# Optimization experiments

Hardware: AMD Instinct MI355X
Metric: run time of the kernel (lower is better)

## Reference

```python
import jax, jax.numpy as jnp
import numpy as np

N = 100_000   # num nodes
E = 3_200_000 # num directed edges (before self-loops)
NEG_SLOPE = 0.2


def setup_inputs() -> dict:
    key = jax.random.key(0)
    ks = jax.random.split(key, 12)
    x = jax.random.normal(ks[0], (N, 2), jnp.float32)
    edge_index = jax.random.randint(ks[1], (2, E), 0, N, dtype=jnp.int32)
    # GATConv(2, 16): lin weight [2,16] (no bias), att_src/att_dst [16], out bias [16]
    W1 = jax.random.normal(ks[2], (2, 16), jnp.float32) * (1.0 / np.sqrt(2.0))
    a_src1 = jax.random.normal(ks[3], (16,), jnp.float32) * 0.25
    a_dst1 = jax.random.normal(ks[4], (16,), jnp.float32) * 0.25
    b1 = jnp.zeros((16,), jnp.float32)
    # GATConv(16, 64)
    W2 = jax.random.normal(ks[5], (16, 64), jnp.float32) * (1.0 / np.sqrt(16.0))
    a_src2 = jax.random.normal(ks[6], (64,), jnp.float32) * 0.125
    a_dst2 = jax.random.normal(ks[7], (64,), jnp.float32) * 0.125
    b2 = jnp.zeros((64,), jnp.float32)
    return {"x": x, "edge_index": edge_index,
            "W1": W1, "a_src1": a_src1, "a_dst1": a_dst1, "b1": b1,
            "W2": W2, "a_src2": a_src2, "a_dst2": a_dst2, "b2": b2}


def _gat_layer(x, src, dst, W, a_src, a_dst, b):
    # x: [N, Fin]; src/dst: [E'] (self-loops included). Single head, PyG GATConv math.
    h = x @ W                                        # [N, Fout]
    alpha_s = h @ a_src                              # [N]
    alpha_d = h @ a_dst                              # [N]
    e = jax.nn.leaky_relu(alpha_s[src] + alpha_d[dst], NEG_SLOPE)  # [E']
    # segment softmax over incoming edges of each dst node
    m = jax.ops.segment_max(e, dst, num_segments=N)
    m = jnp.where(jnp.isfinite(m), m, 0.0)           # nodes always have a self-loop, but be safe
    p = jnp.exp(e - m[dst])
    s = jax.ops.segment_sum(p, dst, num_segments=N)
    alpha = p / s[dst]                               # [E']
    out = jax.ops.segment_sum(alpha[:, None] * h[src], dst, num_segments=N)  # [N, Fout]
    return out + b


def reference(x, edge_index, W1, a_src1, a_dst1, b1, W2, a_src2, a_dst2, b2):
    # PyG GATConv adds self-loops by default
    loops = jnp.arange(N, dtype=edge_index.dtype)
    src = jnp.concatenate([edge_index[0], loops])
    dst = jnp.concatenate([edge_index[1], loops])
    h = jax.nn.relu(_gat_layer(x, src, dst, W1, a_src1, a_dst1, b1))
    h = jax.nn.relu(_gat_layer(h, src, dst, W2, a_src2, a_dst2, b2))
    return h
```

## Files before the change

### kernel.cpp

```cpp
#include <hip/hip_runtime.h>

#define NNODES 100000
#define NEDGES 3200000
#define ETOT   (NEDGES + NNODES)
#define NEG_SLOPE 0.2f
#define LOG2E 1.4426950408889634f

#define NPB 64
#define NBUCK ((NNODES + NPB - 1) / NPB)
#define NCHUNK 256
#define CHUNK_E ((ETOT + NCHUNK - 1) / NCHUNK)
#define M2 (NBUCK * NCHUNK)
#define NSB2 ((M2 + 511) / 512)
#define FS_CAP 4096

__device__ __forceinline__ unsigned short f2bf(float f) {
    unsigned u = __float_as_uint(f);
    u += 0x7FFFu + ((u >> 16) & 1u);
    return (unsigned short)(u >> 16);
}
__device__ __forceinline__ float bf2f(unsigned short h) {
    return __uint_as_float(((unsigned)h) << 16);
}

__device__ __forceinline__ void edge_sd(int e, const int* __restrict__ ei, int& s, int& d) {
    if (e < NEDGES) { s = ei[e]; d = ei[NEDGES + e]; }
    else            { s = e - NEDGES; d = s; }
}

__device__ __forceinline__ float lrelu(float v) {
    return v > 0.0f ? v : NEG_SLOPE * v;
}

__device__ __forceinline__ float edge_w(float z) {
    return __builtin_amdgcn_exp2f(lrelu(z));
}

template<int CTRL>
__device__ __forceinline__ float dpp_mov(float v) {
    return __int_as_float(__builtin_amdgcn_mov_dpp(__float_as_int(v), CTRL, 0xF, 0xF, true));
}
template<int CTRL>
__device__ __forceinline__ float dpp_add(float v) { return v + dpp_mov<CTRL>(v); }
template<int IMM>
__device__ __forceinline__ float swz(float v) {
    return __int_as_float(__builtin_amdgcn_ds_swizzle(__float_as_int(v), IMM));
}
__device__ __forceinline__ float swz16_add(float v) { return v + swz<0x401F>(v); }
__device__ __forceinline__ float row16_sum(float v) {
    v = dpp_add<0x121>(v);
    v = dpp_add<0x122>(v);
    v = dpp_add<0x124>(v);
    v = dpp_add<0x128>(v);
    return v;
}
__device__ __forceinline__ float half32_sum(float v) {
    v = row16_sum(v);
    v = swz16_add(v);
    return v;
}


__global__ void chunk_hist(const int* __restrict__ ei, int* __restrict__ H) {
    __shared__ int h[NBUCK];
    int c = blockIdx.x;
    for (int i = threadIdx.x; i < NBUCK; i += blockDim.x) h[i] = 0;
    __syncthreads();
    int lo = c * CHUNK_E, hi = lo + CHUNK_E; if (hi > ETOT) hi = ETOT;
    for (int e = lo + threadIdx.x; e < hi; e += blockDim.x) {
        int d = (e < NEDGES) ? ei[NEDGES + e] : (e - NEDGES);
        atomicAdd(&h[d >> 6], 1);
    }
    __syncthreads();
    for (int i = threadIdx.x; i < NBUCK; i += blockDim.x) H[c * NBUCK + i] = h[i];
}

__global__ void cscan_local(const int* __restrict__ H, int* __restrict__ off,
                            int* __restrict__ bsum2) {
    __shared__ int arr[512];
    int blk = blockIdx.x, t = threadIdx.x;
    int i = blk * 512 + t;
    int v = (i < M2) ? H[(i & (NCHUNK - 1)) * NBUCK + (i >> 8)] : 0;
    arr[t] = v;
    __syncthreads();
    for (int o = 1; o < 512; o <<= 1) {
        int u = (t >= o) ? arr[t - o] : 0;
        __syncthreads();
        arr[t] += u;
        __syncthreads();
    }
    if (i < M2) off[i] = arr[t] - v;
    if (t == 511) bsum2[blk] = arr[t];
}

__global__ void cscan_bsum(const int* __restrict__ bsum2, int* __restrict__ boff2) {
    __shared__ int arr[1024];
    int t = threadIdx.x;
    int v = (t < NSB2) ? bsum2[t] : 0;
    arr[t] = v;
    __syncthreads();
    for (int o = 1; o < 1024; o <<= 1) {
        int u = (t >= o) ? arr[t - o] : 0;
        __syncthreads();
        arr[t] += u;
        __syncthreads();
    }
    if (t < NSB2) boff2[t] = arr[t] - v;
}

__global__ __launch_bounds__(1024)
void chunk_scatter(const int* __restrict__ ei, const int* __restrict__ off,
                   const int* __restrict__ boff2, const int* __restrict__ H,
                   int* __restrict__ pairs) {
    __shared__ int plds[CHUNK_E];
    __shared__ unsigned short blds[CHUNK_E];
    __shared__ int sc[2048];
    __shared__ int lcur[NBUCK];
    __shared__ int gbase[NBUCK];
    int c = blockIdx.x, t = threadIdx.x;
    for (int b = t; b < 2048; b += 1024) sc[b] = (b < NBUCK) ? H[c * NBUCK + b] : 0;
    __syncthreads();
    for (int o = 1; o < 2048; o <<= 1) {
        int i1 = t + 1024;
        int v0 = (t >= o) ? sc[t - o] : 0;
        int v1 = (i1 >= o) ? sc[i1 - o] : 0;
        __syncthreads();
        sc[t] += v0; sc[i1] += v1;
        __syncthreads();
    }
    for (int b = t; b < NBUCK; b += 1024) {
        int excl = (b == 0) ? 0 : sc[b - 1];
        lcur[b]  = excl;
        gbase[b] = off[b * NCHUNK + c] + boff2[b >> 1] - excl;
    }
    __syncthreads();
    int lo = c * CHUNK_E, hi = lo + CHUNK_E; if (hi > ETOT) hi = ETOT;
    int n = hi - lo;
    for (int e = lo + t; e < hi; e += 1024) {
        int s, d; edge_sd(e, ei, s, d);
        int b = d >> 6;
        int slot = atomicAdd(&lcur[b], 1);
        plds[slot] = ((d & 63) << 17) | s;
        blds[slot] = (unsigned short)b;
    }
    __syncthreads();
    for (int i = t; i < n; i += 1024)
        pairs[gbase[blds[i]] + i] = plds[i];
}

__global__ __launch_bounds__(512)
void fine_sort2(const int* __restrict__ off, const int* __restrict__ boff2,
                const int* __restrict__ pairs,
                int* __restrict__ row_start, int* __restrict__ csr_src) {
    __shared__ int sp[FS_CAP];
    __shared__ int arr[NPB];
    __shared__ int cur[NPB];
    int b = blockIdx.x;
    int t = threadIdx.x;
    int base = off[b * NCHUNK] + boff2[b >> 1];
    int bend = (b == NBUCK - 1) ? ETOT : off[(b + 1) * NCHUNK] + boff2[(b + 1) >> 1];
    int n = bend - base;
    if (t < NPB) arr[t] = 0;
    __syncthreads();
    bool fits = (n <= FS_CAP);
    if (fits) {
        for (int i = t; i < n; i += 512) {
            int p = pairs[base + i];
            sp[i] = p;
            atomicAdd(&arr[p >> 17], 1);
        }
    } else {
        for (int i = t; i < n; i += 512)
            atomicAdd(&arr[pairs[base + i] >> 17], 1);
    }
    __syncthreads();
    int v = (t < NPB) ? arr[t] : 0;
    __syncthreads();
    for (int o = 1; o < NPB; o <<= 1) {
        int u = (t < NPB && t >= o) ? arr[t - o] : 0;
        __syncthreads();
        if (t < NPB) arr[t] += u;
        __syncthreads();
    }
    if (t < NPB) {
        int node = b * NPB + t;
        int start = base + arr[t] - v;
        cur[t] = start;
        if (node < NNODES) row_start[node] = start;
    }
    if (b == NBUCK - 1 && t == 0) row_start[NNODES] = ETOT;
    __syncthreads();
    if (fits) {
        for (int i = t; i < n; i += 512) {
            int p = sp[i];
            int slot = atomicAdd(&cur[p >> 17], 1);
            csr_src[slot] = p & 0x1FFFF;
        }
    } else {
        for (int i = t; i < n; i += 512) {
            int p = pairs[base + i];
            int slot = atomicAdd(&cur[p >> 17], 1);
            csr_src[slot] = p & 0x1FFFF;
        }
    }
}

__global__ void prep(const float* __restrict__ W1, const float* __restrict__ as1,
                     const float* __restrict__ ad1, const float* __restrict__ W2,
                     const float* __restrict__ as2, const float* __restrict__ ad2,
                     float* __restrict__ cvec) {
    int t = threadIdx.x;
    if (t < 2) {
        float s = 0.f, d = 0.f;
        for (int f = 0; f < 16; ++f) { s += W1[t * 16 + f] * as1[f]; d += W1[t * 16 + f] * ad1[f]; }
        cvec[t] = s * LOG2E; cvec[2 + t] = d * LOG2E;
    }
    if (t < 16) {
        float s = 0.f, d = 0.f;
        for (int f = 0; f < 64; ++f) { s += W2[t * 64 + f] * as2[f]; d += W2[t * 64 + f] * ad2[f]; }
        cvec[4 + t] = s * LOG2E; cvec[20 + t] = d * LOG2E;
    }
}

__global__ void alpha1(const float* __restrict__ x, const float* __restrict__ cvec,
                       float4* __restrict__ nrec1, float* __restrict__ ad_) {
    int n = blockIdx.x * blockDim.x + threadIdx.x;
    if (n >= NNODES) return;
    float2 xv = ((const float2*)x)[n];
    float as = xv.x * cvec[0] + xv.y * cvec[1];
    ad_[n] = xv.x * cvec[2] + xv.y * cvec[3];
    nrec1[n] = make_float4(xv.x, xv.y, as, 0.f);
}

__global__ void agg_l1(const int* __restrict__ row_start, const int* __restrict__ csr_src,
                       const float4* __restrict__ nrec1, const float* __restrict__ ad_,
                       const float* __restrict__ W1, const float* __restrict__ b1,
                       const float* __restrict__ cvec,
                       float* __restrict__ nrec2, float* __restrict__ ad2_) {
    int wave = threadIdx.x >> 6;
    int half = (threadIdx.x >> 5) & 1;
    int hlane = threadIdx.x & 31;
    int node = blockIdx.x * 8 + wave * 2 + half;
    int base = row_start[node], end = row_start[node + 1];
    float adv = ad_[node];
    float a0 = 0.f, a1 = 0.f, ss = 0.f;
    for (int i = base + hlane; i < end; i += 32) {
        int sj = csr_src[i];
        float4 r = nrec1[sj];
        float w = edge_w(r.z + adv);
        ss += w;
        a0 += w * r.x;
        a1 += w * r.y;
    }
    a0 = half32_sum(a0); a1 = half32_sum(a1); ss = half32_sum(ss);
    int f = hlane & 15;
    float v = (a0 * W1[f] + a1 * W1[16 + f]) / ss + b1[f];
    float vr = v > 0.f ? v : 0.f;
    unsigned short* grow = (unsigned short*)(nrec2 + (size_t)node * 16);
    if (hlane < 16) grow[hlane] = f2bf(vr);
    float s2 = vr * cvec[4 + f];
    float d2 = vr * cvec[20 + f];
    s2 = row16_sum(s2); d2 = row16_sum(d2);
    if (hlane == 0) {
        nrec2[(size_t)node * 16 + 8] = s2;
        ad2_[node] = d2;
    }
}

__global__ void agg_l2(const int* __restrict__ row_start, const int* __restrict__ csr_src,
                       const float* __restrict__ nrec2, const float* __restrict__ ad_,
                       const float* __restrict__ W2, const float* __restrict__ b2,
                       float* __restrict__ out) {
    __shared__ float tot[4][2][16];
    int wave = threadIdx.x >> 6;
    int half = (threadIdx.x >> 5) & 1;
    int hlane = threadIdx.x & 31;
    int node = blockIdx.x * 8 + wave * 2 + half;
    int base = row_start[node], end = row_start[node + 1];
    float adv = ad_[node];
    float acc[16];
#pragma unroll
    for (int k = 0; k < 16; ++k) acc[k] = 0.f;
    float ss = 0.f;
    for (int i = base + hlane; i < end; i += 32) {
        int sj = csr_src[i];
        const float* recf = nrec2 + (size_t)sj * 16;
        const uint4* rec4 = (const uint4*)recf;
        uint4 u0 = rec4[0], u1 = rec4[1];
        float as2v = recf[8];
        float w = edge_w(as2v + adv);
        ss += w;
        unsigned uu[8] = {u0.x, u0.y, u0.z, u0.w, u1.x, u1.y, u1.z, u1.w};
#pragma unroll
        for (int j = 0; j < 8; ++j) {
            acc[2 * j]     += w * __uint_as_float(uu[j] << 16);
            acc[2 * j + 1] += w * __uint_as_float(uu[j] & 0xFFFF0000u);
        }
    }
#pragma unroll
    for (int j = 0; j < 8; ++j) {
        float keep = (hlane & 1) ? acc[2 * j + 1] : acc[2 * j];
        float send = (hlane & 1) ? acc[2 * j]     : acc[2 * j + 1];
        acc[j] = keep + dpp_mov<0xB1>(send);
    }
#pragma unroll
    for (int j = 0; j < 4; ++j) {
        float keep = (hlane & 2) ? acc[2 * j + 1] : acc[2 * j];
        float send = (hlane & 2) ? acc[2 * j]     : acc[2 * j + 1];
        acc[j] = keep + dpp_mov<0x4E>(send);
    }
#pragma unroll
    for (int j = 0; j < 2; ++j) {
        float keep = (hlane & 4) ? acc[2 * j + 1] : acc[2 * j];
        float send = (hlane & 4) ? acc[2 * j]     : acc[2 * j + 1];
        acc[j] = keep + swz<0x101F>(send);
    }
    float r;
    {
        float keep = (hlane & 8) ? acc[1] : acc[0];
        float send = (hlane & 8) ? acc[0] : acc[1];
        r = keep + swz<0x201F>(send);
    }
    r = swz16_add(r);
    float st = half32_sum(ss);
    if (hlane < 16) tot[wave][half][hlane] = r;
    float o0 = 0.f, o1 = 0.f;
#pragma unroll
    for (int k = 0; k < 16; ++k) {
        float t = tot[wave][half][k];
        o0 += t * W2[k * 64 + hlane];
        o1 += t * W2[k * 64 + 32 + hlane];
    }
    float inv = 1.0f / st;
    o0 = o0 * inv + b2[hlane];
    o1 = o1 * inv + b2[32 + hlane];
    out[(size_t)node * 64 + hlane]      = o0 > 0.f ? o0 : 0.f;
    out[(size_t)node * 64 + 32 + hlane] = o1 > 0.f ? o1 : 0.f;
}

extern "C" void kernel_launch(void* const* d_in, const int* in_sizes, int n_in,
                              void* d_out, int out_size, void* d_ws, size_t ws_size,
                              hipStream_t stream) {
    const float* x     = (const float*)d_in[0];
    const int*   ei    = (const int*)  d_in[1];
    const float* W1    = (const float*)d_in[2];
    const float* as1w  = (const float*)d_in[3];
    const float* ad1w  = (const float*)d_in[4];
    const float* b1    = (const float*)d_in[5];
    const float* W2    = (const float*)d_in[6];
    const float* as2w  = (const float*)d_in[7];
    const float* ad2w  = (const float*)d_in[8];
    const float* b2    = (const float*)d_in[9];
    float* out = (float*)d_out;

    int* row_start = (int*)d_ws;
    int* csr_src   = row_start + (NNODES + 4);
    float* nrec2   = (float*)(csr_src + ETOT);
    float* adb     = nrec2 + (size_t)NNODES * 16;
    float* ad2b    = adb + NNODES;
    float* cvec    = ad2b + NNODES;
    int* pairs     = (int*)(cvec + 64);
    int* H         = pairs + ETOT;
    int* off       = H + M2;
    int* bsum2     = off + M2;
    int* boff2     = bsum2 + 1024;
    float4* nrec1  = (float4*)(boff2 + 1024);

    const int B = 256;
    const int NB = (NNODES + B - 1) / B;

    chunk_hist<<<NCHUNK, 1024, 0, stream>>>(ei, H);
    cscan_local<<<NSB2, 512, 0, stream>>>(H, off, bsum2);
    cscan_bsum<<<1, 1024, 0, stream>>>(bsum2, boff2);
    chunk_scatter<<<NCHUNK, 1024, 0, stream>>>(ei, off, boff2, H, pairs);
    fine_sort2<<<NBUCK, 512, 0, stream>>>(off, boff2, pairs, row_start, csr_src);

    prep<<<1, 64, 0, stream>>>(W1, as1w, ad1w, W2, as2w, ad2w, cvec);

    alpha1<<<NB, B, 0, stream>>>(x, cvec, nrec1, adb);
    agg_l1<<<NNODES / 8, B, 0, stream>>>(row_start, csr_src, nrec1, adb, W1, b1,
                                         cvec, nrec2, ad2b);

    agg_l2<<<NNODES / 8, B, 0, stream>>>(row_start, csr_src, nrec2, ad2b, W2, b2, out);
}
```

Measured before the change: 215.9 us.

## Fuse fine CSR sort with layer-1 aggregation in one kernel

Merges the per-bucket fine sort and the layer-1 attention aggregation into a single kernel. Each block sorts its 64-node bucket, keeps the sorted source indices in shared memory, and aggregates layer 1 directly from LDS instead of re-reading csr_src from global memory. This drops one kernel launch and a global round trip of the edge list, at the cost of doubled LDS use per block (lower occupancy) and fewer, larger blocks for the aggregation phase.

```diff
diff --git a/kernel.cpp b/kernel.cpp
--- a/kernel.cpp
+++ b/kernel.cpp
@@ -148,63 +148,6 @@
         pairs[gbase[blds[i]] + i] = plds[i];
 }
 
-__global__ __launch_bounds__(512)
-void fine_sort2(const int* __restrict__ off, const int* __restrict__ boff2,
-                const int* __restrict__ pairs,
-                int* __restrict__ row_start, int* __restrict__ csr_src) {
-    __shared__ int sp[FS_CAP];
-    __shared__ int arr[NPB];
-    __shared__ int cur[NPB];
-    int b = blockIdx.x;
-    int t = threadIdx.x;
-    int base = off[b * NCHUNK] + boff2[b >> 1];
-    int bend = (b == NBUCK - 1) ? ETOT : off[(b + 1) * NCHUNK] + boff2[(b + 1) >> 1];
-    int n = bend - base;
-    if (t < NPB) arr[t] = 0;
-    __syncthreads();
-    bool fits = (n <= FS_CAP);
-    if (fits) {
-        for (int i = t; i < n; i += 512) {
-            int p = pairs[base + i];
-            sp[i] = p;
-            atomicAdd(&arr[p >> 17], 1);
-        }
-    } else {
-        for (int i = t; i < n; i += 512)
-            atomicAdd(&arr[pairs[base + i] >> 17], 1);
-    }
-    __syncthreads();
-    int v = (t < NPB) ? arr[t] : 0;
-    __syncthreads();
-    for (int o = 1; o < NPB; o <<= 1) {
-        int u = (t < NPB && t >= o) ? arr[t - o] : 0;
-        __syncthreads();
-        if (t < NPB) arr[t] += u;
-        __syncthreads();
-    }
-    if (t < NPB) {
-        int node = b * NPB + t;
-        int start = base + arr[t] - v;
-        cur[t] = start;
-        if (node < NNODES) row_start[node] = start;
-    }
-    if (b == NBUCK - 1 && t == 0) row_start[NNODES] = ETOT;
-    __syncthreads();
-    if (fits) {
-        for (int i = t; i < n; i += 512) {
-            int p = sp[i];
-            int slot = atomicAdd(&cur[p >> 17], 1);
-            csr_src[slot] = p & 0x1FFFF;
-        }
-    } else {
-        for (int i = t; i < n; i += 512) {
-            int p = pairs[base + i];
-            int slot = atomicAdd(&cur[p >> 17], 1);
-            csr_src[slot] = p & 0x1FFFF;
-        }
-    }
-}
-
 __global__ void prep(const float* __restrict__ W1, const float* __restrict__ as1,
                      const float* __restrict__ ad1, const float* __restrict__ W2,
                      const float* __restrict__ as2, const float* __restrict__ ad2,
@@ -232,38 +175,112 @@
     nrec1[n] = make_float4(xv.x, xv.y, as, 0.f);
 }
 
-__global__ void agg_l1(const int* __restrict__ row_start, const int* __restrict__ csr_src,
-                       const float4* __restrict__ nrec1, const float* __restrict__ ad_,
-                       const float* __restrict__ W1, const float* __restrict__ b1,
-                       const float* __restrict__ cvec,
-                       float* __restrict__ nrec2, float* __restrict__ ad2_) {
-    int wave = threadIdx.x >> 6;
-    int half = (threadIdx.x >> 5) & 1;
-    int hlane = threadIdx.x & 31;
-    int node = blockIdx.x * 8 + wave * 2 + half;
-    int base = row_start[node], end = row_start[node + 1];
-    float adv = ad_[node];
-    float a0 = 0.f, a1 = 0.f, ss = 0.f;
-    for (int i = base + hlane; i < end; i += 32) {
-        int sj = csr_src[i];
-        float4 r = nrec1[sj];
-        float w = edge_w(r.z + adv);
-        ss += w;
-        a0 += w * r.x;
-        a1 += w * r.y;
-    }
-    a0 = half32_sum(a0); a1 = half32_sum(a1); ss = half32_sum(ss);
-    int f = hlane & 15;
-    float v = (a0 * W1[f] + a1 * W1[16 + f]) / ss + b1[f];
-    float vr = v > 0.f ? v : 0.f;
-    unsigned short* grow = (unsigned short*)(nrec2 + (size_t)node * 16);
-    if (hlane < 16) grow[hlane] = f2bf(vr);
-    float s2 = vr * cvec[4 + f];
-    float d2 = vr * cvec[20 + f];
-    s2 = row16_sum(s2); d2 = row16_sum(d2);
-    if (hlane == 0) {
-        nrec2[(size_t)node * 16 + 8] = s2;
-        ad2_[node] = d2;
+__global__ __launch_bounds__(512)
+void fine_agg1(const int* __restrict__ off, const int* __restrict__ boff2,
+               const int* __restrict__ pairs,
+               const float4* __restrict__ nrec1, const float* __restrict__ ad_,
+               const float* __restrict__ W1, const float* __restrict__ b1,
+               const float* __restrict__ cvec,
+               int* __restrict__ row_start, int* __restrict__ csr_src,
+               float* __restrict__ nrec2, float* __restrict__ ad2_) {
+    __shared__ int sp[FS_CAP];
+    __shared__ int spc[FS_CAP];
+    __shared__ int arr[NPB];
+    __shared__ int cur[NPB];
+    __shared__ int lstart[NPB + 1];
+    int b = blockIdx.x;
+    int t = threadIdx.x;
+    int base = off[b * NCHUNK] + boff2[b >> 1];
+    int bend = (b == NBUCK - 1) ? ETOT : off[(b + 1) * NCHUNK] + boff2[(b + 1) >> 1];
+    int n = bend - base;
+    if (t < NPB) arr[t] = 0;
+    __syncthreads();
+    bool fits = (n <= FS_CAP);
+    if (fits) {
+        for (int i = t; i < n; i += 512) {
+            int p = pairs[base + i];
+            sp[i] = p;
+            atomicAdd(&arr[p >> 17], 1);
+        }
+    } else {
+        for (int i = t; i < n; i += 512)
+            atomicAdd(&arr[pairs[base + i] >> 17], 1);
+    }
+    __syncthreads();
+    int v = (t < NPB) ? arr[t] : 0;
+    __syncthreads();
+    for (int o = 1; o < NPB; o <<= 1) {
+        int u = (t < NPB && t >= o) ? arr[t - o] : 0;
+        __syncthreads();
+        if (t < NPB) arr[t] += u;
+        __syncthreads();
+    }
+    if (t < NPB) {
+        int node = b * NPB + t;
+        int start = base + arr[t] - v;
+        cur[t] = start;
+        lstart[t] = start;
+        if (node < NNODES) row_start[node] = start;
+    }
+    if (t == 0) lstart[NPB] = bend;
+    if (b == NBUCK - 1 && t == 0) row_start[NNODES] = ETOT;
+    __syncthreads();
+    if (fits) {
+        for (int i = t; i < n; i += 512) {
+            int p = sp[i];
+            int slot = atomicAdd(&cur[p >> 17], 1);
+            int src = p & 0x1FFFF;
+            csr_src[slot] = src;
+            spc[slot - base] = src;
+        }
+    } else {
+        for (int i = t; i < n; i += 512) {
+            int p = pairs[base + i];
+            int slot = atomicAdd(&cur[p >> 17], 1);
+            csr_src[slot] = p & 0x1FFFF;
+        }
+        __threadfence_block();
+    }
+    __syncthreads();
+    int wave = t >> 6;
+    int half = (t >> 5) & 1;
+    int hlane = t & 31;
+#pragma unroll
+    for (int pass = 0; pass < 4; ++pass) {
+        int ln = pass * 16 + wave * 2 + half;
+        int node = b * NPB + ln;
+        if (node >= NNODES) continue;
+        int nbase = lstart[ln], nend = lstart[ln + 1];
+        float adv = ad_[node];
+        float a0 = 0.f, a1 = 0.f, ss = 0.f;
+        if (fits) {
+            for (int i = nbase + hlane; i < nend; i += 32) {
+                int sj = spc[i - base];
+                float4 r = nrec1[sj];
+                float w = edge_w(r.z + adv);
+                ss += w; a0 += w * r.x; a1 += w * r.y;
+            }
+        } else {
+            for (int i = nbase + hlane; i < nend; i += 32) {
+                int sj = csr_src[i];
+                float4 r = nrec1[sj];
+                float w = edge_w(r.z + adv);
+                ss += w; a0 += w * r.x; a1 += w * r.y;
+            }
+        }
+        a0 = half32_sum(a0); a1 = half32_sum(a1); ss = half32_sum(ss);
+        int f = hlane & 15;
+        float vv = (a0 * W1[f] + a1 * W1[16 + f]) / ss + b1[f];
+        float vr = vv > 0.f ? vv : 0.f;
+        unsigned short* grow = (unsigned short*)(nrec2 + (size_t)node * 16);
+        if (hlane < 16) grow[hlane] = f2bf(vr);
+        float s2 = vr * cvec[4 + f];
+        float d2 = vr * cvec[20 + f];
+        s2 = row16_sum(s2); d2 = row16_sum(d2);
+        if (hlane == 0) {
+            nrec2[(size_t)node * 16 + 8] = s2;
+            ad2_[node] = d2;
+        }
     }
 }
 
@@ -373,13 +390,12 @@
     cscan_local<<<NSB2, 512, 0, stream>>>(H, off, bsum2);
     cscan_bsum<<<1, 1024, 0, stream>>>(bsum2, boff2);
     chunk_scatter<<<NCHUNK, 1024, 0, stream>>>(ei, off, boff2, H, pairs);
-    fine_sort2<<<NBUCK, 512, 0, stream>>>(off, boff2, pairs, row_start, csr_src);
 
     prep<<<1, 64, 0, stream>>>(W1, as1w, ad1w, W2, as2w, ad2w, cvec);
-
     alpha1<<<NB, B, 0, stream>>>(x, cvec, nrec1, adb);
-    agg_l1<<<NNODES / 8, B, 0, stream>>>(row_start, csr_src, nrec1, adb, W1, b1,
-                                         cvec, nrec2, ad2b);
+
+    fine_agg1<<<NBUCK, 512, 0, stream>>>(off, boff2, pairs, nrec1, adb, W1, b1,
+                                         cvec, row_start, csr_src, nrec2, ad2b);
 
     agg_l2<<<NNODES / 8, B, 0, stream>>>(row_start, csr_src, nrec2, ad2b, W2, b2, out);
 }
```

New measurement: 211.2 us. 2.2% less time.
